# Kernel optimization log

Measured on AMD Instinct MI355X. Metric: run time of the kernel, lower is better.

The kernel has to match this reference:

```python
import jax, jax.numpy as jnp
import numpy as np

B = 4096
NQ = 4  # qubits -> 16-dim state vector


def _make_ops(seed, n_ops):
    # Deterministic stand-in for tq.RandomLayer: random RX/RY/RZ/CRX gates.
    rng = np.random.default_rng(seed)
    ops = []
    for _ in range(n_ops):
        kind = int(rng.integers(0, 4))
        if kind == 3:  # CRX on two distinct wires
            w = rng.choice(NQ, size=2, replace=False)
            ops.append((3, int(w[0]), int(w[1])))
        else:
            ops.append((kind, int(rng.integers(0, NQ)), 0))
    return ops

ENC_OPS = _make_ops(1, 8)    # QuantumPatchEncoder.random_layer (n_ops=8)
QFC_OPS = _make_ops(2, 50)   # QuantumFullyConnectedLayer.random_layer (n_ops=50)

_H = np.array([[1, 1], [1, -1]], np.complex64) * np.complex64(1.0 / np.sqrt(2.0))
_SX = np.array([[1 + 1j, 1 - 1j], [1 - 1j, 1 + 1j]], np.complex64) * np.complex64(0.5)
_CNOT = np.array([[1, 0, 0, 0], [0, 1, 0, 0], [0, 0, 0, 1], [0, 0, 1, 0]], np.complex64)


def _rx(t):
    c = jnp.cos(t / 2) + 0j
    s = -1j * jnp.sin(t / 2)
    return jnp.stack([jnp.stack([c, s], -1), jnp.stack([s, c], -1)], -2)


def _ry(t):
    c = jnp.cos(t / 2) + 0j
    s = jnp.sin(t / 2) + 0j
    return jnp.stack([jnp.stack([c, -s], -1), jnp.stack([s, c], -1)], -2)


def _rz(t):
    e0 = jnp.exp(-1j * t / 2)
    e1 = jnp.exp(1j * t / 2)
    z = jnp.zeros_like(e0)
    return jnp.stack([jnp.stack([e0, z], -1), jnp.stack([z, e1], -1)], -2)


def _crx(t):
    return jnp.eye(4, dtype=jnp.complex64).at[2:, 2:].set(_rx(t))


def _apply1(state, U, w):
    # state: (B, 2,2,2,2); U: (2,2) or per-sample (B,2,2)
    state = jnp.moveaxis(state, w + 1, -1)
    if U.ndim == 3:
        state = jnp.einsum('b...i,bji->b...j', state, U)
    else:
        state = jnp.einsum('...i,ji->...j', state, U)
    return jnp.moveaxis(state, -1, w + 1)


def _apply2(state, U, w0, w1):
    state = jnp.moveaxis(state, (w0 + 1, w1 + 1), (-2, -1))
    shp = state.shape
    state = state.reshape(shp[:-2] + (4,)) @ U.T
    return jnp.moveaxis(state.reshape(shp), (-2, -1), (w0 + 1, w1 + 1))


def _random_layer(state, ops, params):
    for i, (kind, w0, w1) in enumerate(ops):
        t = params[i]
        if kind == 0:
            state = _apply1(state, _rx(t), w0)
        elif kind == 1:
            state = _apply1(state, _ry(t), w0)
        elif kind == 2:
            state = _apply1(state, _rz(t), w0)
        else:
            state = _apply2(state, _crx(t), w0, w1)
    return state


def _measure_z(state):
    # <Z> on each wire from |amp|^2 marginals
    probs = state.real ** 2 + state.imag ** 2
    exps = []
    for w in range(NQ):
        axes = tuple(a for a in range(1, NQ + 1) if a != w + 1)
        m = probs.sum(axes)  # (B, 2)
        exps.append(m[:, 0] - m[:, 1])
    return jnp.stack(exps, 1)


def _conv(x, W, b):
    y = jax.lax.conv_general_dilated(x, W, (1, 1), 'SAME',
                                     dimension_numbers=('NCHW', 'OIHW', 'NCHW'))
    return y + b[None, :, None, None]


def _pool(x):
    return jax.lax.reduce_window(x, -jnp.inf, jax.lax.max,
                                 (1, 1, 2, 2), (1, 1, 2, 2), 'VALID')


def setup_inputs() -> dict:
    key = jax.random.key(0)
    ks = jax.random.split(key, 8)
    f = lambda k, shp, fan: jax.random.normal(k, shp, jnp.float32) / np.float32(np.sqrt(fan))
    two_pi = float(2 * np.pi)
    return {
        'x': jax.random.uniform(ks[0], (B, 1, 32, 32), jnp.float32),
        'conv1_w': f(ks[1], (8, 1, 3, 3), 9),
        'conv1_b': jnp.zeros((8,), jnp.float32),
        'conv2_w': f(ks[2], (16, 8, 3, 3), 72),
        'conv2_b': jnp.zeros((16,), jnp.float32),
        'enc_params': jax.random.uniform(ks[3], (8,), jnp.float32, 0.0, two_pi),
        'qfc_rand_params': jax.random.uniform(ks[4], (50,), jnp.float32, 0.0, two_pi),
        'qfc_params': jax.random.uniform(ks[5], (4,), jnp.float32, 0.0, two_pi),
        'bn_gamma': jnp.ones((4,), jnp.float32),
        'bn_beta': jnp.zeros((4,), jnp.float32),
        'fc_w': f(ks[6], (10, 68), 68),
        'fc_b': jnp.zeros((10,), jnp.float32),
    }


def reference(x, conv1_w, conv1_b, conv2_w, conv2_b, enc_params, qfc_rand_params,
              qfc_params, bn_gamma, bn_beta, fc_w, fc_b):
    # CNN feature extractor
    h = _pool(jax.nn.relu(_conv(x, conv1_w, conv1_b)))
    h = _pool(jax.nn.relu(_conv(h, conv2_w, conv2_b)))  # (B, 16, 8, 8)
    b = h.shape[0]
    pm = h.mean(1)  # channel-mean, (B, 8, 8)
    # 2x2 patches, row-major within patch, scanning r then c -> (B, 16, 4)
    patches = pm.reshape(b, 4, 2, 4, 2).transpose(0, 1, 3, 2, 4).reshape(b, 16, 4)

    # Encoder: fresh |0000> per patch (GeneralEncoder resets state); batch all
    # B*16 patch circuits together instead of looping.
    data = patches.reshape(b * 16, 4)
    state = jnp.zeros((b * 16, 16), jnp.complex64).at[:, 0].set(1.0)
    state = state.reshape(b * 16, 2, 2, 2, 2)
    for w in range(NQ):
        state = _apply1(state, _ry(data[:, w]), w)
    state = _random_layer(state, ENC_OPS, enc_params)
    qfeat = _measure_z(state).reshape(b, 64)  # (B, 16*4)

    # QFC operates on the state left by the LAST patch (as in the original)
    s = state.reshape(b, 16, 2, 2, 2, 2)[:, 15]
    s = _random_layer(s, QFC_OPS, qfc_rand_params)
    s = _apply1(s, _rx(qfc_params[0]), 0)
    s = _apply1(s, _ry(qfc_params[1]), 1)
    s = _apply1(s, _rz(qfc_params[2]), 3)
    s = _apply2(s, _crx(qfc_params[3]), 0, 2)
    s = _apply1(s, jnp.asarray(_H), 3)
    s = _apply1(s, jnp.asarray(_SX), 2)
    s = _apply2(s, jnp.asarray(_CNOT), 3, 0)
    q = _measure_z(s)  # (B, 4)

    # BatchNorm1d(4), training-mode (batch stats, biased var)
    mu = q.mean(0)
    var = q.var(0)
    q = (q - mu) / jnp.sqrt(var + 1e-5) * bn_gamma + bn_beta

    feats = jnp.concatenate([qfeat, q], 1)  # (B, 68)
    logits = feats @ fc_w.T + fc_b
    return jax.nn.log_softmax(logits, -1)
```

## Files before the change

### kernel.cpp

```cpp
#include <hip/hip_runtime.h>
#include <cstdint>

namespace crng {

typedef unsigned __int128 u128;

struct PCG {
    u128 state, inc;
    bool has32;
    uint32_t buf32;
};

constexpr u128 PCG_MULT = (((u128)2549297995355413924ULL) << 64) | (u128)4865540595714422341ULL;

constexpr uint64_t pcg_next64(PCG& g) {
    g.state = g.state * PCG_MULT + g.inc;
    uint64_t hi = (uint64_t)(g.state >> 64), lo = (uint64_t)g.state;
    unsigned rot = (unsigned)(g.state >> 122) & 63u;
    uint64_t v = hi ^ lo;
    return (v >> rot) | (v << ((64u - rot) & 63u));
}

constexpr uint32_t pcg_next32(PCG& g) {
    if (g.has32) { g.has32 = false; return g.buf32; }
    uint64_t n = pcg_next64(g);
    g.has32 = true;
    g.buf32 = (uint32_t)(n >> 32);
    return (uint32_t)n;
}

constexpr uint32_t hashmix(uint32_t& hc, uint32_t v) {
    v ^= hc; hc *= 0x931e8875u; v *= hc; v ^= v >> 16; return v;
}
constexpr uint32_t mixf(uint32_t x, uint32_t y) {
    uint32_t r = 0xca01f9ddu * x - 0x4973f715u * y;
    r ^= r >> 16;
    return r;
}

constexpr PCG seed_pcg(uint32_t entropy) {
    uint32_t pool[4] = {0, 0, 0, 0};
    uint32_t hc = 0x43b0d7e5u;
    pool[0] = hashmix(hc, entropy);
    for (int i = 1; i < 4; ++i) pool[i] = hashmix(hc, 0u);
    for (int s = 0; s < 4; ++s)
        for (int d = 0; d < 4; ++d)
            if (s != d) pool[d] = mixf(pool[d], hashmix(hc, pool[s]));

    uint32_t hb = 0x8b51f9ddu;
    uint32_t w[8] = {0, 0, 0, 0, 0, 0, 0, 0};
    for (int i = 0; i < 8; ++i) {
        uint32_t dv = pool[i & 3];
        dv ^= hb; hb *= 0x58f38dedu; dv *= hb; dv ^= dv >> 16;
        w[i] = dv;
    }
    uint64_t w64[4] = {0, 0, 0, 0};
    for (int i = 0; i < 4; ++i)
        w64[i] = (uint64_t)w[2 * i] | ((uint64_t)w[2 * i + 1] << 32);

    u128 initstate = (((u128)w64[0]) << 64) | (u128)w64[1];
    u128 initseq   = (((u128)w64[2]) << 64) | (u128)w64[3];
    PCG g = {};
    g.state = 0;
    g.inc = (initseq << 1) | (u128)1;
    g.state = g.state * PCG_MULT + g.inc;
    g.state += initstate;
    g.state = g.state * PCG_MULT + g.inc;
    g.has32 = false;
    g.buf32 = 0;
    return g;
}

constexpr uint32_t lemire32(PCG& g, uint32_t rng) {
    uint64_t rng_excl = (uint64_t)rng + 1;
    uint64_t m = (uint64_t)pcg_next32(g) * rng_excl;
    uint32_t leftover = (uint32_t)m;
    if (leftover < (uint32_t)rng_excl) {
        uint32_t threshold = (uint32_t)((uint64_t)(0xFFFFFFFFu - rng) % rng_excl);
        while (leftover < threshold) {
            m = (uint64_t)pcg_next32(g) * rng_excl;
            leftover = (uint32_t)m;
        }
    }
    return (uint32_t)(m >> 32);
}

struct Ops {
    int enc[8];
    int qfc[50];
};

constexpr void fill_ops(PCG& g, int n, int* out) {
    for (int i = 0; i < n; ++i) {
        uint32_t kind = lemire32(g, 3);
        uint32_t w0 = 0, w1 = 0;
        if (kind == 3) {
            uint32_t v2 = lemire32(g, 2);
            uint32_t v3 = lemire32(g, 3);
            uint32_t a0 = v2;
            uint32_t a1 = (v3 == v2) ? 3u : v3;
            uint32_t j = lemire32(g, 1);
            if (j == 0) { uint32_t t = a0; a0 = a1; a1 = t; }
            w0 = a0; w1 = a1;
        } else {
            w0 = lemire32(g, 3);
        }
        out[i] = (int)((kind << 4) | (w0 << 2) | w1);
    }
}

constexpr Ops make_ops_ct() {
    Ops o = {};
    PCG g1 = seed_pcg(1u);
    fill_ops(g1, 8, o.enc);
    PCG g2 = seed_pcg(2u);
    fill_ops(g2, 50, o.qfc);
    return o;
}

}

constexpr crng::Ops kOps = crng::make_ops_ct();

typedef _Float16 half8 __attribute__((ext_vector_type(8)));
typedef float float4v __attribute__((ext_vector_type(4)));

#define XS_STRIDE 24
#define XS_PLANE  (34 * XS_STRIDE)
#define XS_TOT    (2 * XS_PLANE)
#define H1F_ROW   (18 * 8)

template<int KIND, int W0, int W1>
__device__ __forceinline__ void gate_ct(float (&ur)[16], float (&ui)[16],
                                        float ch, float sh)
{
    constexpr bool CTRL = (KIND == 3 || KIND == 6);
    constexpr int STT = CTRL ? (8 >> W1) : (8 >> W0);
    constexpr int STC = CTRL ? (8 >> W0) : 0;
#pragma unroll
    for (int k0 = 0; k0 < 16; ++k0) {
        if (k0 & STT) continue;
        if (STC != 0 && !(k0 & STC)) continue;
        const int k1 = k0 | STT;
        float x0r = ur[k0], x0i = ui[k0], x1r = ur[k1], x1i = ui[k1];
        if constexpr (KIND == 0 || KIND == 3) {
            ur[k0] = ch * x0r + sh * x1i;  ui[k0] = ch * x0i - sh * x1r;
            ur[k1] = sh * x0i + ch * x1r;  ui[k1] = -sh * x0r + ch * x1i;
        } else if constexpr (KIND == 1) {
            ur[k0] = ch * x0r - sh * x1r;  ui[k0] = ch * x0i - sh * x1i;
            ur[k1] = sh * x0r + ch * x1r;  ui[k1] = sh * x0i + ch * x1i;
        } else if constexpr (KIND == 2) {
            ur[k0] = ch * x0r + sh * x0i;  ui[k0] = ch * x0i - sh * x0r;
            ur[k1] = ch * x1r - sh * x1i;  ui[k1] = ch * x1i + sh * x1r;
        } else if constexpr (KIND == 4) {
            constexpr float RH = 0.70710678118654752f;
            ur[k0] = RH * (x0r + x1r);  ui[k0] = RH * (x0i + x1i);
            ur[k1] = RH * (x0r - x1r);  ui[k1] = RH * (x0i - x1i);
        } else if constexpr (KIND == 5) {
            ur[k0] = 0.5f * (x0r + x1r) - 0.5f * x0i + 0.5f * x1i;
            ui[k0] = 0.5f * (x0i + x1i) + 0.5f * x0r - 0.5f * x1r;
            ur[k1] = 0.5f * (x0r + x1r) + 0.5f * x0i - 0.5f * x1i;
            ui[k1] = 0.5f * (x0i + x1i) - 0.5f * x0r + 0.5f * x1r;
        } else {
            ur[k0] = x1r; ui[k0] = x1i;
            ur[k1] = x0r; ui[k1] = x0i;
        }
    }
}

template<int I>
__device__ __forceinline__ void run_enc(float (&ur)[16], float (&ui)[16],
                                        const float* ch, const float* sh)
{
    if constexpr (I < 8) {
        constexpr int op = kOps.enc[I];
        gate_ct<(op >> 4) & 7, (op >> 2) & 3, op & 3>(ur, ui, ch[I], sh[I]);
        run_enc<I + 1>(ur, ui, ch, sh);
    }
}

template<int I>
__device__ __forceinline__ void run_qfc(float (&ur)[16], float (&ui)[16],
                                        const float* ch, const float* sh)
{
    if constexpr (I < 50) {
        constexpr int op = kOps.qfc[I];
        gate_ct<(op >> 4) & 7, (op >> 2) & 3, op & 3>(ur, ui, ch[I], sh[I]);
        run_qfc<I + 1>(ur, ui, ch, sh);
    }
}

__global__ __launch_bounds__(256, 4) void cnn_enc_kernel(
    const float* __restrict__ x, const float* __restrict__ w1,
    const float* __restrict__ b1, const float* __restrict__ w2,
    const float* __restrict__ b2, const float* __restrict__ encp,
    float* __restrict__ qfeat, float* __restrict__ sstate,
    float* __restrict__ stats, int* __restrict__ bar)
{
    __shared__ float xs[XS_TOT];
    __shared__ __align__(16) _Float16 h1f[18 * H1F_ROW];
    __shared__ __align__(16) _Float16 Ahalf[9 * 16 * 8];
    __shared__ float w1s[72], b1s[8], b2s[16];
    __shared__ float pm_lds[64];
    __shared__ float chsE[8], shsE[8];

    const int tid = threadIdx.x;
    const int b = blockIdx.x;
    const float* xb = x + (size_t)b * 1024;

    for (int k = tid; k < XS_TOT; k += 256) xs[k] = 0.f;
    for (int k = tid; k < 18 * H1F_ROW; k += 256) h1f[k] = (_Float16)0.f;
    for (int e = tid; e < 1152; e += 256) {
        int uv = e >> 7, m = (e >> 3) & 15, ci = e & 7;
        Ahalf[e] = (_Float16)w2[m * 72 + ci * 9 + uv];
    }
    if (tid < 72) w1s[tid] = w1[tid];
    if (tid < 8) b1s[tid] = b1[tid];
    if (tid < 16) b2s[tid] = b2[tid];
    if (tid < 8) {
        float t = encp[tid];
        chsE[tid] = cosf(0.5f * t);
        shsE[tid] = sinf(0.5f * t);
    }
    if (b == 0 && tid < 8) stats[tid] = 0.f;
    if (b == 0 && tid == 8) *bar = 0;
    __syncthreads();

    {
        const int r = tid >> 3, m = tid & 7;
        float4 v = *(const float4*)(xb + (size_t)tid * 4);
        float* d0p = &xs[(r + 1) * XS_STRIDE + 2 * m];
        float* d1p = &xs[XS_PLANE + (r + 1) * XS_STRIDE + 2 * m];
        d0p[0] = v.x;
        d1p[1] = v.y;
        d0p[1] = v.z;
        d1p[2] = v.w;
    }
    __syncthreads();

    {
        const int i = tid >> 4, j = tid & 15;
        float patch[4][4];
#pragma unroll
        for (int u = 0; u < 4; ++u) {
            int r = 2 * i + u;
            const float* ev = &xs[r * XS_STRIDE + j];
            const float* od = &xs[XS_PLANE + r * XS_STRIDE + j];
            patch[u][0] = od[0];
            patch[u][1] = ev[0];
            patch[u][2] = od[1];
            patch[u][3] = ev[1];
        }
        half8 hv;
#pragma unroll
        for (int c = 0; c < 8; ++c) {
            float m = -3.4e38f;
#pragma unroll
            for (int di = 0; di < 2; ++di)
#pragma unroll
                for (int dj = 0; dj < 2; ++dj) {
                    float acc = b1s[c];
#pragma unroll
                    for (int u = 0; u < 3; ++u)
#pragma unroll
                        for (int v = 0; v < 3; ++v)
                            acc += w1s[c * 9 + u * 3 + v] * patch[di + u][dj + v];
                    m = fmaxf(m, acc);
                }
            hv[c] = (_Float16)fmaxf(m, 0.f);
        }
        *(half8*)&h1f[(i + 1) * H1F_ROW + (j + 1) * 8] = hv;
    }
    __syncthreads();

    {
        const int w = tid >> 6;
        const int lane = tid & 63;
        const int pj = lane & 15;
        const int quad = lane >> 4;

        half8 afrag[9];
#pragma unroll
        for (int uv = 0; uv < 9; ++uv) {
            half8 a = {};
            if (quad == 0) a = *(const half8*)&Ahalf[(uv * 16 + pj) * 8];
            afrag[uv] = a;
        }

        float4v acc[4];
#pragma unroll
        for (int tl = 0; tl < 4; ++tl) {
            float4v c;
#pragma unroll
            for (int r = 0; r < 4; ++r) c[r] = b2s[4 * quad + r];
            acc[tl] = c;
        }

#pragma unroll
        for (int tl = 0; tl < 4; ++tl) {
            const int t = 4 * w + tl;
#pragma unroll
            for (int u = 0; u < 3; ++u) {
#pragma unroll
                for (int v = 0; v < 3; ++v) {
                    half8 bf = *(const half8*)&h1f[(t + u) * H1F_ROW + (pj + v) * 8];
                    acc[tl] = __builtin_amdgcn_mfma_f32_16x16x32_f16(
                        afrag[u * 3 + v], bf, acc[tl], 0, 0, 0);
                }
            }
        }

#pragma unroll
        for (int p = 0; p < 2; ++p) {
            float4v m1;
#pragma unroll
            for (int r = 0; r < 4; ++r)
                m1[r] = fmaxf(acc[2 * p][r], acc[2 * p + 1][r]);
            float s = 0.f;
#pragma unroll
            for (int r = 0; r < 4; ++r) {
                float o = __shfl_xor((float)m1[r], 1, 64);
                float mv = fmaxf(fmaxf(m1[r], o), 0.f);
                s += mv;
            }
            s += __shfl_xor(s, 16, 64);
            s += __shfl_xor(s, 32, 64);
            if (quad == 0 && !(pj & 1)) {
                const int i2 = 2 * w + p, j2 = pj >> 1;
                pm_lds[i2 * 8 + j2] = s * (1.f / 16.f);
            }
        }
    }
    __syncthreads();

    if (tid < 16) {
        const int p = tid, pr = p >> 2, pc = p & 3;
        float d0 = pm_lds[(2 * pr) * 8 + 2 * pc];
        float d1 = pm_lds[(2 * pr) * 8 + 2 * pc + 1];
        float d2 = pm_lds[(2 * pr + 1) * 8 + 2 * pc];
        float d3 = pm_lds[(2 * pr + 1) * 8 + 2 * pc + 1];
        float f0c = cosf(0.5f * d0), f0s = sinf(0.5f * d0);
        float f1c = cosf(0.5f * d1), f1s = sinf(0.5f * d1);
        float f2c = cosf(0.5f * d2), f2s = sinf(0.5f * d2);
        float f3c = cosf(0.5f * d3), f3s = sinf(0.5f * d3);

        float ur[16], ui[16];
#pragma unroll
        for (int k = 0; k < 16; ++k) {
            float v = ((k & 8) ? f0s : f0c);
            v *= ((k & 4) ? f1s : f1c);
            v *= ((k & 2) ? f2s : f2c);
            v *= ((k & 1) ? f3s : f3c);
            ur[k] = v;
            ui[k] = 0.f;
        }
        run_enc<0>(ur, ui, chsE, shsE);

        float qv[4] = {0.f, 0.f, 0.f, 0.f};
#pragma unroll
        for (int k = 0; k < 16; ++k) {
            float pk = ur[k] * ur[k] + ui[k] * ui[k];
            qv[0] += (k & 8) ? -pk : pk;
            qv[1] += (k & 4) ? -pk : pk;
            qv[2] += (k & 2) ? -pk : pk;
            qv[3] += (k & 1) ? -pk : pk;
        }
        *(float4*)(qfeat + (size_t)b * 64 + p * 4) =
            make_float4(qv[0], qv[1], qv[2], qv[3]);

        if (p == 15) {
            float4* sp = (float4*)(sstate + (size_t)b * 32);
#pragma unroll
            for (int i = 0; i < 4; ++i)
                sp[i] = make_float4(ur[4 * i], ur[4 * i + 1], ur[4 * i + 2], ur[4 * i + 3]);
#pragma unroll
            for (int i = 0; i < 4; ++i)
                sp[4 + i] = make_float4(ui[4 * i], ui[4 * i + 1], ui[4 * i + 2], ui[4 * i + 3]);
        }
    }
}

__global__ __launch_bounds__(256) void tail_kernel(
    const float* __restrict__ sstate, const float* __restrict__ qfeat,
    const float* __restrict__ qfcr, const float* __restrict__ qfcp,
    const float* __restrict__ gam, const float* __restrict__ bet,
    const float* __restrict__ fcw, const float* __restrict__ fcb,
    float* __restrict__ stats, int* __restrict__ bar,
    float* __restrict__ out, int Bv, int NBlk)
{
    __shared__ float chs[54], shs[54];
    __shared__ float Wf[680];
    __shared__ float bfs[10], st8[8], ga[4], be[4];
    __shared__ float rstat[32];

    const int tid = threadIdx.x;
    if (tid < 54) {
        float t = (tid < 50) ? qfcr[tid] : qfcp[tid - 50];
        chs[tid] = cosf(0.5f * t);
        shs[tid] = sinf(0.5f * t);
    }
    for (int k = tid; k < 680; k += 256) Wf[k] = fcw[k];
    if (tid < 10) bfs[tid] = fcb[tid];
    if (tid < 4) { ga[tid] = gam[tid]; be[tid] = bet[tid]; }
    __syncthreads();

    const int b = blockIdx.x * 256 + tid;
    float qq[4] = {0.f, 0.f, 0.f, 0.f};

    if (b < Bv) {
        float ur[16], ui[16];
        const float4* sp = (const float4*)(sstate + (size_t)b * 32);
#pragma unroll
        for (int i = 0; i < 4; ++i) {
            float4 v = sp[i];
            ur[4 * i] = v.x; ur[4 * i + 1] = v.y; ur[4 * i + 2] = v.z; ur[4 * i + 3] = v.w;
        }
#pragma unroll
        for (int i = 0; i < 4; ++i) {
            float4 v = sp[4 + i];
            ui[4 * i] = v.x; ui[4 * i + 1] = v.y; ui[4 * i + 2] = v.z; ui[4 * i + 3] = v.w;
        }

        run_qfc<0>(ur, ui, chs, shs);
        gate_ct<0, 0, 0>(ur, ui, chs[50], shs[50]);
        gate_ct<1, 1, 0>(ur, ui, chs[51], shs[51]);
        gate_ct<2, 3, 0>(ur, ui, chs[52], shs[52]);
        gate_ct<3, 0, 2>(ur, ui, chs[53], shs[53]);
        gate_ct<4, 3, 0>(ur, ui, 0.f, 0.f);
        gate_ct<5, 2, 0>(ur, ui, 0.f, 0.f);
        gate_ct<6, 3, 0>(ur, ui, 0.f, 0.f);

#pragma unroll
        for (int k = 0; k < 16; ++k) {
            float pk = ur[k] * ur[k] + ui[k] * ui[k];
            qq[0] += (k & 8) ? -pk : pk;
            qq[1] += (k & 4) ? -pk : pk;
            qq[2] += (k & 2) ? -pk : pk;
            qq[3] += (k & 1) ? -pk : pk;
        }
    }

    {
        const int lane = tid & 63, wv = tid >> 6;
#pragma unroll
        for (int q = 0; q < 8; ++q) {
            float v = (q < 4) ? qq[q] : qq[q - 4] * qq[q - 4];
            v += __shfl_xor(v, 1, 64);
            v += __shfl_xor(v, 2, 64);
            v += __shfl_xor(v, 4, 64);
            v += __shfl_xor(v, 8, 64);
            v += __shfl_xor(v, 16, 64);
            v += __shfl_xor(v, 32, 64);
            if (lane == 0) rstat[q * 4 + wv] = v;
        }
        __syncthreads();
        if (tid < 8)
            atomicAdd(&stats[tid], rstat[tid * 4] + rstat[tid * 4 + 1] +
                                   rstat[tid * 4 + 2] + rstat[tid * 4 + 3]);
    }

    __syncthreads();
    if (tid == 0) {
        __threadfence();
        atomicAdd(bar, 1);
        while (atomicAdd(bar, 0) < NBlk)
            __builtin_amdgcn_s_sleep(8);
    }
    __syncthreads();

    if (tid < 8) st8[tid] = atomicAdd(&stats[tid], 0.f);
    __syncthreads();

    if (b >= Bv) return;

    const float invB = 1.f / (float)Bv;

    float logit[10];
#pragma unroll
    for (int k = 0; k < 10; ++k) logit[k] = bfs[k];

    const float* qf = qfeat + (size_t)b * 64;
#pragma unroll
    for (int j4 = 0; j4 < 16; ++j4) {
        float4 v = *(const float4*)(qf + 4 * j4);
#pragma unroll
        for (int k = 0; k < 10; ++k) {
            const float* wr = &Wf[k * 68 + 4 * j4];
            logit[k] += v.x * wr[0] + v.y * wr[1] + v.z * wr[2] + v.w * wr[3];
        }
    }
#pragma unroll
    for (int w = 0; w < 4; ++w) {
        float mu = st8[w] * invB;
        float var = st8[4 + w] * invB - mu * mu;
        float v = (qq[w] - mu) / sqrtf(var + 1e-5f) * ga[w] + be[w];
#pragma unroll
        for (int k = 0; k < 10; ++k) logit[k] += v * Wf[k * 68 + 64 + w];
    }

    float m = logit[0];
#pragma unroll
    for (int k = 1; k < 10; ++k) m = fmaxf(m, logit[k]);
    float sum = 0.f;
#pragma unroll
    for (int k = 0; k < 10; ++k) sum += expf(logit[k] - m);
    float lse = logf(sum);
#pragma unroll
    for (int k = 0; k < 10; ++k) out[(size_t)b * 10 + k] = logit[k] - m - lse;
}

extern "C" void kernel_launch(void* const* d_in, const int* in_sizes, int n_in,
                              void* d_out, int out_size, void* d_ws, size_t ws_size,
                              hipStream_t stream)
{
    const float* x    = (const float*)d_in[0];
    const float* w1   = (const float*)d_in[1];
    const float* b1   = (const float*)d_in[2];
    const float* w2   = (const float*)d_in[3];
    const float* b2   = (const float*)d_in[4];
    const float* encp = (const float*)d_in[5];
    const float* qfcr = (const float*)d_in[6];
    const float* qfcp = (const float*)d_in[7];
    const float* gam  = (const float*)d_in[8];
    const float* bet  = (const float*)d_in[9];
    const float* fcw  = (const float*)d_in[10];
    const float* fcb  = (const float*)d_in[11];
    float* out = (float*)d_out;

    const int Bv = in_sizes[0] / 1024;

    float* qfeat  = (float*)d_ws;
    float* sstate = qfeat + (size_t)Bv * 64;
    float* stats  = sstate + (size_t)Bv * 32;
    int*   bar    = (int*)(stats + 8);

    cnn_enc_kernel<<<Bv, 256, 0, stream>>>(x, w1, b1, w2, b2, encp,
                                           qfeat, sstate, stats, bar);

    const int nblk = (Bv + 255) / 256;
    tail_kernel<<<nblk, 256, 0, stream>>>(sstate, qfeat, qfcr, qfcp, gam, bet,
                                          fcw, fcb, stats, bar, out, Bv, nblk);
}
```

Baseline: 129.6 us.

## Process four images per CNN block and use per-block BN partial stats

The CNN/encoder kernel now handles four images per block in a loop. Each block loads weights and zero-initialises LDS once and reuses them across the images, and the 64 threads of the quantum encoder stage run together for all four images. The tail kernel now writes per-block BatchNorm partial sums to separate slots and sums them after the grid barrier, replacing the global atomicAdd accumulation. This gives a deterministic summation order and removes the need to zero the stats buffer. In exchange there are 4x fewer blocks, less parallelism and serialized image processing within a block. The allp buffer also caps NBlk at 16.

```diff
diff --git a/kernel.cpp b/kernel.cpp
--- a/kernel.cpp
+++ b/kernel.cpp
@@ -195,18 +195,17 @@
     const float* __restrict__ b1, const float* __restrict__ w2,
     const float* __restrict__ b2, const float* __restrict__ encp,
     float* __restrict__ qfeat, float* __restrict__ sstate,
-    float* __restrict__ stats, int* __restrict__ bar)
+    int* __restrict__ bar, int Bv)
 {
     __shared__ float xs[XS_TOT];
     __shared__ __align__(16) _Float16 h1f[18 * H1F_ROW];
     __shared__ __align__(16) _Float16 Ahalf[9 * 16 * 8];
     __shared__ float w1s[72], b1s[8], b2s[16];
-    __shared__ float pm_lds[64];
+    __shared__ float pm_lds[4][64];
     __shared__ float chsE[8], shsE[8];
 
     const int tid = threadIdx.x;
-    const int b = blockIdx.x;
-    const float* xb = x + (size_t)b * 1024;
+    const int b4 = blockIdx.x * 4;
 
     for (int k = tid; k < XS_TOT; k += 256) xs[k] = 0.f;
     for (int k = tid; k < 18 * H1F_ROW; k += 256) h1f[k] = (_Float16)0.f;
@@ -222,160 +221,170 @@
         chsE[tid] = cosf(0.5f * t);
         shsE[tid] = sinf(0.5f * t);
     }
-    if (b == 0 && tid < 8) stats[tid] = 0.f;
-    if (b == 0 && tid == 8) *bar = 0;
+    if (blockIdx.x == 0 && tid == 8)
+        atomicExch(bar, 0);
     __syncthreads();
 
-    {
-        const int r = tid >> 3, m = tid & 7;
-        float4 v = *(const float4*)(xb + (size_t)tid * 4);
-        float* d0p = &xs[(r + 1) * XS_STRIDE + 2 * m];
-        float* d1p = &xs[XS_PLANE + (r + 1) * XS_STRIDE + 2 * m];
-        d0p[0] = v.x;
-        d1p[1] = v.y;
-        d0p[1] = v.z;
-        d1p[2] = v.w;
-    }
-    __syncthreads();
-
-    {
-        const int i = tid >> 4, j = tid & 15;
-        float patch[4][4];
-#pragma unroll
-        for (int u = 0; u < 4; ++u) {
-            int r = 2 * i + u;
-            const float* ev = &xs[r * XS_STRIDE + j];
-            const float* od = &xs[XS_PLANE + r * XS_STRIDE + j];
-            patch[u][0] = od[0];
-            patch[u][1] = ev[0];
-            patch[u][2] = od[1];
-            patch[u][3] = ev[1];
-        }
-        half8 hv;
-#pragma unroll
-        for (int c = 0; c < 8; ++c) {
-            float m = -3.4e38f;
-#pragma unroll
-            for (int di = 0; di < 2; ++di)
-#pragma unroll
-                for (int dj = 0; dj < 2; ++dj) {
-                    float acc = b1s[c];
-#pragma unroll
-                    for (int u = 0; u < 3; ++u)
-#pragma unroll
-                        for (int v = 0; v < 3; ++v)
-                            acc += w1s[c * 9 + u * 3 + v] * patch[di + u][dj + v];
-                    m = fmaxf(m, acc);
+    for (int img = 0; img < 4; ++img) {
+        const int bimg = b4 + img;
+        const float* xb = x + (size_t)((bimg < Bv) ? bimg : (Bv - 1)) * 1024;
+
+        {
+            const int r = tid >> 3, m = tid & 7;
+            float4 v = *(const float4*)(xb + (size_t)tid * 4);
+            float* d0p = &xs[(r + 1) * XS_STRIDE + 2 * m];
+            float* d1p = &xs[XS_PLANE + (r + 1) * XS_STRIDE + 2 * m];
+            d0p[0] = v.x;
+            d1p[1] = v.y;
+            d0p[1] = v.z;
+            d1p[2] = v.w;
+        }
+        __syncthreads();
+
+        {
+            const int i = tid >> 4, j = tid & 15;
+            float patch[4][4];
+#pragma unroll
+            for (int u = 0; u < 4; ++u) {
+                int r = 2 * i + u;
+                const float* ev = &xs[r * XS_STRIDE + j];
+                const float* od = &xs[XS_PLANE + r * XS_STRIDE + j];
+                patch[u][0] = od[0];
+                patch[u][1] = ev[0];
+                patch[u][2] = od[1];
+                patch[u][3] = ev[1];
+            }
+            half8 hv;
+#pragma unroll
+            for (int c = 0; c < 8; ++c) {
+                float m = -3.4e38f;
+#pragma unroll
+                for (int di = 0; di < 2; ++di)
+#pragma unroll
+                    for (int dj = 0; dj < 2; ++dj) {
+                        float acc = b1s[c];
+#pragma unroll
+                        for (int u = 0; u < 3; ++u)
+#pragma unroll
+                            for (int v = 0; v < 3; ++v)
+                                acc += w1s[c * 9 + u * 3 + v] * patch[di + u][dj + v];
+                        m = fmaxf(m, acc);
+                    }
+                hv[c] = (_Float16)fmaxf(m, 0.f);
+            }
+            *(half8*)&h1f[(i + 1) * H1F_ROW + (j + 1) * 8] = hv;
+        }
+        __syncthreads();
+
+        {
+            const int w = tid >> 6;
+            const int lane = tid & 63;
+            const int pj = lane & 15;
+            const int quad = lane >> 4;
+
+            half8 afrag[9];
+#pragma unroll
+            for (int uv = 0; uv < 9; ++uv) {
+                half8 a = {};
+                if (quad == 0) a = *(const half8*)&Ahalf[(uv * 16 + pj) * 8];
+                afrag[uv] = a;
+            }
+
+            float4v acc[4];
+#pragma unroll
+            for (int tl = 0; tl < 4; ++tl) {
+                float4v c;
+#pragma unroll
+                for (int r = 0; r < 4; ++r) c[r] = b2s[4 * quad + r];
+                acc[tl] = c;
+            }
+
+#pragma unroll
+            for (int tl = 0; tl < 4; ++tl) {
+                const int t = 4 * w + tl;
+#pragma unroll
+                for (int u = 0; u < 3; ++u) {
+#pragma unroll
+                    for (int v = 0; v < 3; ++v) {
+                        half8 bf = *(const half8*)&h1f[(t + u) * H1F_ROW + (pj + v) * 8];
+                        acc[tl] = __builtin_amdgcn_mfma_f32_16x16x32_f16(
+                            afrag[u * 3 + v], bf, acc[tl], 0, 0, 0);
+                    }
                 }
-            hv[c] = (_Float16)fmaxf(m, 0.f);
-        }
-        *(half8*)&h1f[(i + 1) * H1F_ROW + (j + 1) * 8] = hv;
-    }
-    __syncthreads();
-
-    {
-        const int w = tid >> 6;
-        const int lane = tid & 63;
-        const int pj = lane & 15;
-        const int quad = lane >> 4;
-
-        half8 afrag[9];
-#pragma unroll
-        for (int uv = 0; uv < 9; ++uv) {
-            half8 a = {};
-            if (quad == 0) a = *(const half8*)&Ahalf[(uv * 16 + pj) * 8];
-            afrag[uv] = a;
-        }
-
-        float4v acc[4];
-#pragma unroll
-        for (int tl = 0; tl < 4; ++tl) {
-            float4v c;
-#pragma unroll
-            for (int r = 0; r < 4; ++r) c[r] = b2s[4 * quad + r];
-            acc[tl] = c;
-        }
-
-#pragma unroll
-        for (int tl = 0; tl < 4; ++tl) {
-            const int t = 4 * w + tl;
-#pragma unroll
-            for (int u = 0; u < 3; ++u) {
-#pragma unroll
-                for (int v = 0; v < 3; ++v) {
-                    half8 bf = *(const half8*)&h1f[(t + u) * H1F_ROW + (pj + v) * 8];
-                    acc[tl] = __builtin_amdgcn_mfma_f32_16x16x32_f16(
-                        afrag[u * 3 + v], bf, acc[tl], 0, 0, 0);
+            }
+
+#pragma unroll
+            for (int p = 0; p < 2; ++p) {
+                float4v m1;
+#pragma unroll
+                for (int r = 0; r < 4; ++r)
+                    m1[r] = fmaxf(acc[2 * p][r], acc[2 * p + 1][r]);
+                float s = 0.f;
+#pragma unroll
+                for (int r = 0; r < 4; ++r) {
+                    float o = __shfl_xor((float)m1[r], 1, 64);
+                    float mv = fmaxf(fmaxf(m1[r], o), 0.f);
+                    s += mv;
                 }
-            }
-        }
-
-#pragma unroll
-        for (int p = 0; p < 2; ++p) {
-            float4v m1;
-#pragma unroll
-            for (int r = 0; r < 4; ++r)
-                m1[r] = fmaxf(acc[2 * p][r], acc[2 * p + 1][r]);
-            float s = 0.f;
-#pragma unroll
-            for (int r = 0; r < 4; ++r) {
-                float o = __shfl_xor((float)m1[r], 1, 64);
-                float mv = fmaxf(fmaxf(m1[r], o), 0.f);
-                s += mv;
-            }
-            s += __shfl_xor(s, 16, 64);
-            s += __shfl_xor(s, 32, 64);
-            if (quad == 0 && !(pj & 1)) {
-                const int i2 = 2 * w + p, j2 = pj >> 1;
-                pm_lds[i2 * 8 + j2] = s * (1.f / 16.f);
-            }
-        }
-    }
-    __syncthreads();
-
-    if (tid < 16) {
-        const int p = tid, pr = p >> 2, pc = p & 3;
-        float d0 = pm_lds[(2 * pr) * 8 + 2 * pc];
-        float d1 = pm_lds[(2 * pr) * 8 + 2 * pc + 1];
-        float d2 = pm_lds[(2 * pr + 1) * 8 + 2 * pc];
-        float d3 = pm_lds[(2 * pr + 1) * 8 + 2 * pc + 1];
-        float f0c = cosf(0.5f * d0), f0s = sinf(0.5f * d0);
-        float f1c = cosf(0.5f * d1), f1s = sinf(0.5f * d1);
-        float f2c = cosf(0.5f * d2), f2s = sinf(0.5f * d2);
-        float f3c = cosf(0.5f * d3), f3s = sinf(0.5f * d3);
-
-        float ur[16], ui[16];
-#pragma unroll
-        for (int k = 0; k < 16; ++k) {
-            float v = ((k & 8) ? f0s : f0c);
-            v *= ((k & 4) ? f1s : f1c);
-            v *= ((k & 2) ? f2s : f2c);
-            v *= ((k & 1) ? f3s : f3c);
-            ur[k] = v;
-            ui[k] = 0.f;
-        }
-        run_enc<0>(ur, ui, chsE, shsE);
-
-        float qv[4] = {0.f, 0.f, 0.f, 0.f};
-#pragma unroll
-        for (int k = 0; k < 16; ++k) {
-            float pk = ur[k] * ur[k] + ui[k] * ui[k];
-            qv[0] += (k & 8) ? -pk : pk;
-            qv[1] += (k & 4) ? -pk : pk;
-            qv[2] += (k & 2) ? -pk : pk;
-            qv[3] += (k & 1) ? -pk : pk;
-        }
-        *(float4*)(qfeat + (size_t)b * 64 + p * 4) =
-            make_float4(qv[0], qv[1], qv[2], qv[3]);
-
-        if (p == 15) {
-            float4* sp = (float4*)(sstate + (size_t)b * 32);
-#pragma unroll
-            for (int i = 0; i < 4; ++i)
-                sp[i] = make_float4(ur[4 * i], ur[4 * i + 1], ur[4 * i + 2], ur[4 * i + 3]);
-#pragma unroll
-            for (int i = 0; i < 4; ++i)
-                sp[4 + i] = make_float4(ui[4 * i], ui[4 * i + 1], ui[4 * i + 2], ui[4 * i + 3]);
+                s += __shfl_xor(s, 16, 64);
+                s += __shfl_xor(s, 32, 64);
+                if (quad == 0 && !(pj & 1)) {
+                    const int i2 = 2 * w + p, j2 = pj >> 1;
+                    pm_lds[img][i2 * 8 + j2] = s * (1.f / 16.f);
+                }
+            }
+        }
+        __syncthreads();
+    }
+
+    if (tid < 64) {
+        const int img = tid >> 4, p = tid & 15;
+        const int bimg = b4 + img;
+        if (bimg < Bv) {
+            const int pr = p >> 2, pc = p & 3;
+            const float* pmi = pm_lds[img];
+            float d0 = pmi[(2 * pr) * 8 + 2 * pc];
+            float d1 = pmi[(2 * pr) * 8 + 2 * pc + 1];
+            float d2 = pmi[(2 * pr + 1) * 8 + 2 * pc];
+            float d3 = pmi[(2 * pr + 1) * 8 + 2 * pc + 1];
+            float f0c = cosf(0.5f * d0), f0s = sinf(0.5f * d0);
+            float f1c = cosf(0.5f * d1), f1s = sinf(0.5f * d1);
+            float f2c = cosf(0.5f * d2), f2s = sinf(0.5f * d2);
+            float f3c = cosf(0.5f * d3), f3s = sinf(0.5f * d3);
+
+            float ur[16], ui[16];
+#pragma unroll
+            for (int k = 0; k < 16; ++k) {
+                float v = ((k & 8) ? f0s : f0c);
+                v *= ((k & 4) ? f1s : f1c);
+                v *= ((k & 2) ? f2s : f2c);
+                v *= ((k & 1) ? f3s : f3c);
+                ur[k] = v;
+                ui[k] = 0.f;
+            }
+            run_enc<0>(ur, ui, chsE, shsE);
+
+            float qv[4] = {0.f, 0.f, 0.f, 0.f};
+#pragma unroll
+            for (int k = 0; k < 16; ++k) {
+                float pk = ur[k] * ur[k] + ui[k] * ui[k];
+                qv[0] += (k & 8) ? -pk : pk;
+                qv[1] += (k & 4) ? -pk : pk;
+                qv[2] += (k & 2) ? -pk : pk;
+                qv[3] += (k & 1) ? -pk : pk;
+            }
+            *(float4*)(qfeat + (size_t)bimg * 64 + p * 4) =
+                make_float4(qv[0], qv[1], qv[2], qv[3]);
+
+            if (p == 15) {
+                float4* sp = (float4*)(sstate + (size_t)bimg * 32);
+#pragma unroll
+                for (int i = 0; i < 4; ++i)
+                    sp[i] = make_float4(ur[4 * i], ur[4 * i + 1], ur[4 * i + 2], ur[4 * i + 3]);
+#pragma unroll
+                for (int i = 0; i < 4; ++i)
+                    sp[4 + i] = make_float4(ui[4 * i], ui[4 * i + 1], ui[4 * i + 2], ui[4 * i + 3]);
+            }
         }
     }
 }
@@ -385,13 +394,14 @@
     const float* __restrict__ qfcr, const float* __restrict__ qfcp,
     const float* __restrict__ gam, const float* __restrict__ bet,
     const float* __restrict__ fcw, const float* __restrict__ fcb,
-    float* __restrict__ stats, int* __restrict__ bar,
+    float* __restrict__ pstat, int* __restrict__ bar,
     float* __restrict__ out, int Bv, int NBlk)
 {
     __shared__ float chs[54], shs[54];
     __shared__ float Wf[680];
     __shared__ float bfs[10], st8[8], ga[4], be[4];
     __shared__ float rstat[32];
+    __shared__ float allp[128];
 
     const int tid = threadIdx.x;
     if (tid < 54) {
@@ -454,9 +464,11 @@
             if (lane == 0) rstat[q * 4 + wv] = v;
         }
         __syncthreads();
-        if (tid < 8)
-            atomicAdd(&stats[tid], rstat[tid * 4] + rstat[tid * 4 + 1] +
-                                   rstat[tid * 4 + 2] + rstat[tid * 4 + 3]);
+        if (tid < 8) {
+            float pv = ((rstat[tid * 4 + 0] + rstat[tid * 4 + 1]) +
+                        rstat[tid * 4 + 2]) + rstat[tid * 4 + 3];
+            atomicExch(&pstat[blockIdx.x * 8 + tid], pv);
+        }
     }
 
     __syncthreads();
@@ -468,7 +480,14 @@
     }
     __syncthreads();
 
-    if (tid < 8) st8[tid] = atomicAdd(&stats[tid], 0.f);
+    if (tid < 8 * NBlk)
+        allp[tid] = atomicAdd(&pstat[tid], 0.f);
+    __syncthreads();
+    if (tid < 8) {
+        float s = 0.f;
+        for (int k = 0; k < NBlk; ++k) s += allp[k * 8 + tid];
+        st8[tid] = s;
+    }
     __syncthreads();
 
     if (b >= Bv) return;
@@ -531,13 +550,14 @@
 
     float* qfeat  = (float*)d_ws;
     float* sstate = qfeat + (size_t)Bv * 64;
-    float* stats  = sstate + (size_t)Bv * 32;
-    int*   bar    = (int*)(stats + 8);
-
-    cnn_enc_kernel<<<Bv, 256, 0, stream>>>(x, w1, b1, w2, b2, encp,
-                                           qfeat, sstate, stats, bar);
-
-    const int nblk = (Bv + 255) / 256;
-    tail_kernel<<<nblk, 256, 0, stream>>>(sstate, qfeat, qfcr, qfcp, gam, bet,
-                                          fcw, fcb, stats, bar, out, Bv, nblk);
-}
+    float* pstat  = sstate + (size_t)Bv * 32;
+    int*   bar    = (int*)(pstat + 128);
+
+    const int nblk1 = (Bv + 3) / 4;
+    cnn_enc_kernel<<<nblk1, 256, 0, stream>>>(x, w1, b1, w2, b2, encp,
+                                              qfeat, sstate, bar, Bv);
+
+    const int nblk2 = (Bv + 255) / 256;
+    tail_kernel<<<nblk2, 256, 0, stream>>>(sstate, qfeat, qfcr, qfcp, gam, bet,
+                                           fcw, fcb, pstat, bar, out, Bv, nblk2);
+}
```

New measurement: 129.0 us. Within noise of the previous version (-0.5%).

## Replace atomic grid barrier with separate QFC and head kernels

Applied to the files above, without the earlier changes.

Splits the tail kernel into a QFC kernel that writes raw Z expectations to workspace and a head kernel that recomputes BatchNorm batch statistics redundantly in every block, then applies the FC layer and log-softmax. This removes the spin-wait grid barrier, the global atomics and the stats/barrier reset in the encoder kernel. In exchange it adds a kernel launch, and each block rereads all 4096x4 raw values and reduces them serially over 256 partials in shared memory.

```diff
diff --git a/kernel.cpp b/kernel.cpp
--- a/kernel.cpp
+++ b/kernel.cpp
@@ -194,8 +194,7 @@
     const float* __restrict__ x, const float* __restrict__ w1,
     const float* __restrict__ b1, const float* __restrict__ w2,
     const float* __restrict__ b2, const float* __restrict__ encp,
-    float* __restrict__ qfeat, float* __restrict__ sstate,
-    float* __restrict__ stats, int* __restrict__ bar)
+    float* __restrict__ qfeat, float* __restrict__ sstate)
 {
     __shared__ float xs[XS_TOT];
     __shared__ __align__(16) _Float16 h1f[18 * H1F_ROW];
@@ -222,8 +221,6 @@
         chsE[tid] = cosf(0.5f * t);
         shsE[tid] = sinf(0.5f * t);
     }
-    if (b == 0 && tid < 8) stats[tid] = 0.f;
-    if (b == 0 && tid == 8) *bar = 0;
     __syncthreads();
 
     {
@@ -380,97 +377,91 @@
     }
 }
 
-__global__ __launch_bounds__(256) void tail_kernel(
-    const float* __restrict__ sstate, const float* __restrict__ qfeat,
-    const float* __restrict__ qfcr, const float* __restrict__ qfcp,
-    const float* __restrict__ gam, const float* __restrict__ bet,
-    const float* __restrict__ fcw, const float* __restrict__ fcb,
-    float* __restrict__ stats, int* __restrict__ bar,
-    float* __restrict__ out, int Bv, int NBlk)
+__global__ __launch_bounds__(256) void qfc_kernel(
+    const float* __restrict__ sstate, const float* __restrict__ qfcr,
+    const float* __restrict__ qfcp, float* __restrict__ qraw, int Bv)
 {
     __shared__ float chs[54], shs[54];
-    __shared__ float Wf[680];
-    __shared__ float bfs[10], st8[8], ga[4], be[4];
-    __shared__ float rstat[32];
-
     const int tid = threadIdx.x;
     if (tid < 54) {
         float t = (tid < 50) ? qfcr[tid] : qfcp[tid - 50];
         chs[tid] = cosf(0.5f * t);
         shs[tid] = sinf(0.5f * t);
     }
+    __syncthreads();
+
+    const int b = blockIdx.x * 256 + tid;
+    if (b >= Bv) return;
+
+    float ur[16], ui[16];
+    const float4* sp = (const float4*)(sstate + (size_t)b * 32);
+#pragma unroll
+    for (int i = 0; i < 4; ++i) {
+        float4 v = sp[i];
+        ur[4 * i] = v.x; ur[4 * i + 1] = v.y; ur[4 * i + 2] = v.z; ur[4 * i + 3] = v.w;
+    }
+#pragma unroll
+    for (int i = 0; i < 4; ++i) {
+        float4 v = sp[4 + i];
+        ui[4 * i] = v.x; ui[4 * i + 1] = v.y; ui[4 * i + 2] = v.z; ui[4 * i + 3] = v.w;
+    }
+
+    run_qfc<0>(ur, ui, chs, shs);
+    gate_ct<0, 0, 0>(ur, ui, chs[50], shs[50]);
+    gate_ct<1, 1, 0>(ur, ui, chs[51], shs[51]);
+    gate_ct<2, 3, 0>(ur, ui, chs[52], shs[52]);
+    gate_ct<3, 0, 2>(ur, ui, chs[53], shs[53]);
+    gate_ct<4, 3, 0>(ur, ui, 0.f, 0.f);
+    gate_ct<5, 2, 0>(ur, ui, 0.f, 0.f);
+    gate_ct<6, 3, 0>(ur, ui, 0.f, 0.f);
+
+    float qq[4] = {0.f, 0.f, 0.f, 0.f};
+#pragma unroll
+    for (int k = 0; k < 16; ++k) {
+        float pk = ur[k] * ur[k] + ui[k] * ui[k];
+        qq[0] += (k & 8) ? -pk : pk;
+        qq[1] += (k & 4) ? -pk : pk;
+        qq[2] += (k & 2) ? -pk : pk;
+        qq[3] += (k & 1) ? -pk : pk;
+    }
+    *(float4*)(qraw + (size_t)b * 4) = make_float4(qq[0], qq[1], qq[2], qq[3]);
+}
+
+__global__ __launch_bounds__(256) void head_kernel(
+    const float* __restrict__ qfeat, const float* __restrict__ qraw,
+    const float* __restrict__ gam, const float* __restrict__ bet,
+    const float* __restrict__ fcw, const float* __restrict__ fcb,
+    float* __restrict__ out, int Bv)
+{
+    __shared__ float Wf[680];
+    __shared__ float bfs[10], ga[4], be[4], st8[8];
+    __shared__ float part[8][256];
+
+    const int tid = threadIdx.x;
     for (int k = tid; k < 680; k += 256) Wf[k] = fcw[k];
     if (tid < 10) bfs[tid] = fcb[tid];
     if (tid < 4) { ga[tid] = gam[tid]; be[tid] = bet[tid]; }
+
+    {
+        float s0 = 0.f, s1 = 0.f, s2 = 0.f, s3 = 0.f;
+        float q0 = 0.f, q1 = 0.f, q2 = 0.f, q3 = 0.f;
+        for (int smp = tid; smp < Bv; smp += 256) {
+            float4 v = *(const float4*)(qraw + (size_t)smp * 4);
+            s0 += v.x; s1 += v.y; s2 += v.z; s3 += v.w;
+            q0 += v.x * v.x; q1 += v.y * v.y; q2 += v.z * v.z; q3 += v.w * v.w;
+        }
+        part[0][tid] = s0; part[1][tid] = s1; part[2][tid] = s2; part[3][tid] = s3;
+        part[4][tid] = q0; part[5][tid] = q1; part[6][tid] = q2; part[7][tid] = q3;
+    }
+    __syncthreads();
+    if (tid < 8) {
+        float s = 0.f;
+        for (int k = 0; k < 256; ++k) s += part[tid][k];
+        st8[tid] = s;
+    }
     __syncthreads();
 
     const int b = blockIdx.x * 256 + tid;
-    float qq[4] = {0.f, 0.f, 0.f, 0.f};
-
-    if (b < Bv) {
-        float ur[16], ui[16];
-        const float4* sp = (const float4*)(sstate + (size_t)b * 32);
-#pragma unroll
-        for (int i = 0; i < 4; ++i) {
-            float4 v = sp[i];
-            ur[4 * i] = v.x; ur[4 * i + 1] = v.y; ur[4 * i + 2] = v.z; ur[4 * i + 3] = v.w;
-        }
-#pragma unroll
-        for (int i = 0; i < 4; ++i) {
-            float4 v = sp[4 + i];
-            ui[4 * i] = v.x; ui[4 * i + 1] = v.y; ui[4 * i + 2] = v.z; ui[4 * i + 3] = v.w;
-        }
-
-        run_qfc<0>(ur, ui, chs, shs);
-        gate_ct<0, 0, 0>(ur, ui, chs[50], shs[50]);
-        gate_ct<1, 1, 0>(ur, ui, chs[51], shs[51]);
-        gate_ct<2, 3, 0>(ur, ui, chs[52], shs[52]);
-        gate_ct<3, 0, 2>(ur, ui, chs[53], shs[53]);
-        gate_ct<4, 3, 0>(ur, ui, 0.f, 0.f);
-        gate_ct<5, 2, 0>(ur, ui, 0.f, 0.f);
-        gate_ct<6, 3, 0>(ur, ui, 0.f, 0.f);
-
-#pragma unroll
-        for (int k = 0; k < 16; ++k) {
-            float pk = ur[k] * ur[k] + ui[k] * ui[k];
-            qq[0] += (k & 8) ? -pk : pk;
-            qq[1] += (k & 4) ? -pk : pk;
-            qq[2] += (k & 2) ? -pk : pk;
-            qq[3] += (k & 1) ? -pk : pk;
-        }
-    }
-
-    {
-        const int lane = tid & 63, wv = tid >> 6;
-#pragma unroll
-        for (int q = 0; q < 8; ++q) {
-            float v = (q < 4) ? qq[q] : qq[q - 4] * qq[q - 4];
-            v += __shfl_xor(v, 1, 64);
-            v += __shfl_xor(v, 2, 64);
-            v += __shfl_xor(v, 4, 64);
-            v += __shfl_xor(v, 8, 64);
-            v += __shfl_xor(v, 16, 64);
-            v += __shfl_xor(v, 32, 64);
-            if (lane == 0) rstat[q * 4 + wv] = v;
-        }
-        __syncthreads();
-        if (tid < 8)
-            atomicAdd(&stats[tid], rstat[tid * 4] + rstat[tid * 4 + 1] +
-                                   rstat[tid * 4 + 2] + rstat[tid * 4 + 3]);
-    }
-
-    __syncthreads();
-    if (tid == 0) {
-        __threadfence();
-        atomicAdd(bar, 1);
-        while (atomicAdd(bar, 0) < NBlk)
-            __builtin_amdgcn_s_sleep(8);
-    }
-    __syncthreads();
-
-    if (tid < 8) st8[tid] = atomicAdd(&stats[tid], 0.f);
-    __syncthreads();
-
     if (b >= Bv) return;
 
     const float invB = 1.f / (float)Bv;
@@ -489,11 +480,14 @@
             logit[k] += v.x * wr[0] + v.y * wr[1] + v.z * wr[2] + v.w * wr[3];
         }
     }
+
+    float4 qr = *(const float4*)(qraw + (size_t)b * 4);
+    float qn[4] = {qr.x, qr.y, qr.z, qr.w};
 #pragma unroll
     for (int w = 0; w < 4; ++w) {
         float mu = st8[w] * invB;
         float var = st8[4 + w] * invB - mu * mu;
-        float v = (qq[w] - mu) / sqrtf(var + 1e-5f) * ga[w] + be[w];
+        float v = (qn[w] - mu) / sqrtf(var + 1e-5f) * ga[w] + be[w];
 #pragma unroll
         for (int k = 0; k < 10; ++k) logit[k] += v * Wf[k * 68 + 64 + w];
     }
@@ -531,13 +525,13 @@
 
     float* qfeat  = (float*)d_ws;
     float* sstate = qfeat + (size_t)Bv * 64;
-    float* stats  = sstate + (size_t)Bv * 32;
-    int*   bar    = (int*)(stats + 8);
+    float* qraw   = sstate + (size_t)Bv * 32;
 
     cnn_enc_kernel<<<Bv, 256, 0, stream>>>(x, w1, b1, w2, b2, encp,
-                                           qfeat, sstate, stats, bar);
+                                           qfeat, sstate);
 
     const int nblk = (Bv + 255) / 256;
-    tail_kernel<<<nblk, 256, 0, stream>>>(sstate, qfeat, qfcr, qfcp, gam, bet,
-                                          fcw, fcb, stats, bar, out, Bv, nblk);
-}
+    qfc_kernel<<<nblk, 256, 0, stream>>>(sstate, qfcr, qfcp, qraw, Bv);
+    head_kernel<<<nblk, 256, 0, stream>>>(qfeat, qraw, gam, bet, fcw, fcb,
+                                          out, Bv);
+}
```

Result: no change. 130.4 us (+0.6%).
